# Optimization experiments

Hardware: AMD Instinct MI355X
Metric: run time of the kernel (lower is better)

Reference implementation:

```python
import jax, jax.numpy as jnp
import numpy as np


def setup_inputs() -> dict:
    key = jax.random.key(0)
    ks = jax.random.split(key, 6)
    B, S, H = 4, 256, 768            # batch, subword seq len, BERT hidden
    N = 128                          # token_num (word-level units)
    HID, L = 1024, 16                # MLP hidden, label count
    all_hidden = jax.random.normal(ks[0], (B, S, H), dtype=jnp.float32)
    starts = jax.random.randint(ks[1], (B, N), 0, S)
    W1 = jax.random.normal(ks[2], (4 * H, HID), dtype=jnp.float32) * 0.02
    b1 = jnp.zeros((HID,), dtype=jnp.float32)
    W2 = jax.random.normal(ks[3], (HID, L), dtype=jnp.float32) * 0.02
    b2 = jnp.zeros((L,), dtype=jnp.float32)
    return {"all_hidden": all_hidden, "starts": starts,
            "W1": W1, "b1": b1, "W2": W2, "b2": b2}


def reference(all_hidden, starts, W1, b1, W2, b2):
    # Span gather: con_repr[b, n, :] = all_hidden[b, starts[b, n], :]
    con = jnp.take_along_axis(all_hidden, starts[:, :, None], axis=1)  # [B, N, H]
    B, N, H = con.shape
    a = jnp.broadcast_to(con[:, :, None, :], (B, N, N, H))  # ext_row
    c = jnp.broadcast_to(con[:, None, :, :], (B, N, N, H))  # ext_column
    table = jnp.concatenate([a, c, a - c, a * c], axis=-1)   # [B, N, N, 4H]
    hid = jnp.tanh(jnp.einsum('bijf,fh->bijh', table, W1) + b1)
    out = jnp.einsum('bijh,hl->bijl', hid, W2) + b2          # [B, N, N, L]
    return out
```

## Files before the change

### kernel.cpp

```cpp
#include <hip/hip_runtime.h>
#include <hip/hip_bf16.h>

typedef __attribute__((ext_vector_type(8))) short short8;
typedef __attribute__((ext_vector_type(8))) unsigned short ushort8;
typedef __attribute__((ext_vector_type(4))) float floatx4;
typedef __attribute__((ext_vector_type(16))) float floatx16;
typedef __attribute__((ext_vector_type(4))) unsigned int uint4v;
typedef __attribute__((ext_vector_type(2))) unsigned int uint2v;

#define DEVINL static __device__ __forceinline__

DEVINL float b2f(unsigned short s){ union{unsigned u; float f;} v; v.u=((unsigned)s)<<16; return v.f; }
DEVINL unsigned fbits(float f){ union{float f; unsigned u;} v; v.f=f; return v.u; }
DEVINL unsigned pack2(float f0, float f1){
  return __builtin_amdgcn_perm(fbits(f1)+0x8000u, fbits(f0)+0x8000u, 0x07060302u);
}
DEVINL float tanh_fast(float v){
  float ax = fabsf(v);
  float ex = __expf(-2.f*ax);
  float th = (1.f - ex)*__builtin_amdgcn_rcpf(1.f + ex);
  return copysignf(th, v);
}

constexpr int Sc=256, Hc=768, Nc=128, HIDc=1024, Lc=16;

__global__ __launch_bounds__(256) void k_gather(const float* __restrict__ AH,
                                                const int* __restrict__ ST,
                                                unsigned short* __restrict__ con){
  int row = blockIdx.x;
  int b = row >> 7;
  int st = ST[row];
  const float* src = AH + ((size_t)(b*Sc + st))*Hc;
  unsigned short* dst = con + (size_t)row*Hc;
  int t = threadIdx.x;
  if (t < 192) {
    float4 v = reinterpret_cast<const float4*>(src)[t];
    uint2v o = { pack2(v.x, v.y), pack2(v.z, v.w) };
    *reinterpret_cast<uint2v*>(dst + 4*t) = o;
  }
}

__global__ __launch_bounds__(256) void k_w1m(const float* __restrict__ W1,
                                             unsigned short* __restrict__ w1mF){
  int sid = blockIdx.x*256 + threadIdx.x;
  int l = sid & 63, kc = (sid >> 6) % 48, ht = sid / (48*64);
  int k = kc*16 + (l >> 5)*8;
  int h = ht*32 + (l & 31);
  const float* wp = W1 + (size_t)(2304 + k)*1024 + h;
  uint4v d;
  d[0] = pack2(wp[0],      wp[1024]);
  d[1] = pack2(wp[2*1024], wp[3*1024]);
  d[2] = pack2(wp[4*1024], wp[5*1024]);
  d[3] = pack2(wp[6*1024], wp[7*1024]);
  *reinterpret_cast<uint4v*>(w1mF + (size_t)sid*8) = d;
}

__global__ __launch_bounds__(256) void k_w2t(const float* __restrict__ W2,
                                             unsigned short* __restrict__ w2F2){
  int gid = blockIdx.x*256 + threadIdx.x;
  int l = gid & 63, chunk = gid >> 6;
  int row = l & 31, s = l >> 5;
  unsigned u[4];
  #pragma unroll
  for (int p = 0; p < 4; ++p) {
    int e0 = 2*p, e1 = 2*p + 1;
    int h0 = chunk*16 + 4*s + (e0 & 3) + 8*(e0 >> 2);
    int h1 = chunk*16 + 4*s + (e1 & 3) + 8*(e1 >> 2);
    float v0 = (row < 16) ? W2[(size_t)h0*Lc + row] : 0.f;
    float v1 = (row < 16) ? W2[(size_t)h1*Lc + row] : 0.f;
    u[p] = pack2(v0, v1);
  }
  uint4v d = { u[0], u[1], u[2], u[3] };
  *reinterpret_cast<uint4v*>(w2F2 + (size_t)gid*8) = d;
}

__global__ __launch_bounds__(256) void k_wpq(const float* __restrict__ W1,
                                             unsigned short* __restrict__ wPQF){
  int sid = blockIdx.x*256 + threadIdx.x;
  int lane = sid & 63, kcq = (sid >> 6) % 24, ht = sid / (24*64);
  int col = lane & 15, seg = lane >> 4;
  int hp = ht*16 + col;
  int kb = kcq*32 + seg*8;
  uint4v d;
  if (hp < 1024) {
    const float* w0 = W1 + (size_t)kb*1024 + hp;
    const float* wd = W1 + (size_t)(1536+kb)*1024 + hp;
    d[0] = pack2(w0[0]+wd[0],           w0[1024]+wd[1024]);
    d[1] = pack2(w0[2*1024]+wd[2*1024], w0[3*1024]+wd[3*1024]);
    d[2] = pack2(w0[4*1024]+wd[4*1024], w0[5*1024]+wd[5*1024]);
    d[3] = pack2(w0[6*1024]+wd[6*1024], w0[7*1024]+wd[7*1024]);
  } else {
    int hq = hp - 1024;
    const float* wc = W1 + (size_t)(768+kb)*1024 + hq;
    const float* wd = W1 + (size_t)(1536+kb)*1024 + hq;
    d[0] = pack2(wc[0]-wd[0],           wc[1024]-wd[1024]);
    d[1] = pack2(wc[2*1024]-wd[2*1024], wc[3*1024]-wd[3*1024]);
    d[2] = pack2(wc[4*1024]-wd[4*1024], wc[5*1024]-wd[5*1024]);
    d[3] = pack2(wc[6*1024]-wd[6*1024], wc[7*1024]-wd[7*1024]);
  }
  *reinterpret_cast<uint4v*>(wPQF + (size_t)sid*8) = d;
}

__global__ __launch_bounds__(256) void k_pq(const unsigned short* __restrict__ con,
                                            const unsigned short* __restrict__ wPQF,
                                            float* __restrict__ P, float* __restrict__ Q){
  int rg = blockIdx.x >> 4, hg = blockIdx.x & 15;
  int t = threadIdx.x, w = t >> 6, lane = t & 63;
  int colh = lane & 15, rseg = lane >> 4;
  floatx4 zero = {0.f,0.f,0.f,0.f};
  floatx4 acc[2][2] = {{zero,zero},{zero,zero}};
  const unsigned short* a0p = con + (size_t)(rg*32 + colh)*Hc + rseg*8;
  const unsigned short* a1p = a0p + 16*Hc;
  const unsigned short* b0p = wPQF + (((size_t)((hg*8 + w*2)*24)) << 9) + (lane << 3);
  const unsigned short* b1p = b0p + (24 << 9);
  #pragma unroll
  for (int kc = 0; kc < 24; ++kc) {
    short8 af0 = *reinterpret_cast<const short8*>(a0p + kc*32);
    short8 af1 = *reinterpret_cast<const short8*>(a1p + kc*32);
    short8 bf0 = *reinterpret_cast<const short8*>(b0p + ((size_t)kc << 9));
    short8 bf1 = *reinterpret_cast<const short8*>(b1p + ((size_t)kc << 9));
    acc[0][0] = __builtin_amdgcn_mfma_f32_16x16x32_bf16(af0, bf0, acc[0][0], 0,0,0);
    acc[0][1] = __builtin_amdgcn_mfma_f32_16x16x32_bf16(af0, bf1, acc[0][1], 0,0,0);
    acc[1][0] = __builtin_amdgcn_mfma_f32_16x16x32_bf16(af1, bf0, acc[1][0], 0,0,0);
    acc[1][1] = __builtin_amdgcn_mfma_f32_16x16x32_bf16(af1, bf1, acc[1][1], 0,0,0);
  }
  #pragma unroll
  for (int m = 0; m < 2; ++m)
    #pragma unroll
    for (int n = 0; n < 2; ++n)
      #pragma unroll
      for (int rr = 0; rr < 4; ++rr) {
        int row = rg*32 + m*16 + rseg*4 + rr;
        int hp = hg*128 + w*32 + n*16 + colh;
        float val = acc[m][n][rr];
        if (hg < 8) P[(size_t)row*HIDc + hp] = val;
        else        Q[(size_t)row*HIDc + (hp - 1024)] = val;
      }
}

__global__ __launch_bounds__(256, 2) void k_main(const unsigned short* __restrict__ con,
    const unsigned short* __restrict__ w1mF, const unsigned short* __restrict__ w2F2,
    const float* __restrict__ P, const float* __restrict__ Q, const float* __restrict__ b1,
    const float* __restrict__ b2v, float* __restrict__ out){
  __shared__ float a_row[768];
  __shared__ float Pi_lds[1024];
  __shared__ __align__(16) unsigned short A_lds[2][4][64][8];
  __shared__ __align__(16) float red[16][64][4];

  int bid = blockIdx.x, jh = bid & 1, bi = bid >> 1;
  int b = bi >> 7, i = bi & 127, bN = b*128;
  int t = threadIdx.x, w = t >> 6, lane = t & 63;
  int col32 = lane & 31, hi5 = lane >> 5;

  int kc2A = t >> 7, jtA = (t >> 6) & 1;
  int jstage = jh*64 + jtA*32 + col32;
  int koffA = kc2A*16 + hi5*8;
  const unsigned short* conA = con + (size_t)(bN + jstage)*Hc + koffA;
  unsigned short* Awr0 = &A_lds[0][kc2A*2 + jtA][lane][0];
  unsigned short* Awr1 = &A_lds[1][kc2A*2 + jtA][lane][0];

  if (t < 96) {
    ushort8 c8 = *reinterpret_cast<const ushort8*>(con + (size_t)(bN + i)*Hc + t*8);
    #pragma unroll
    for (int e = 0; e < 8; ++e) a_row[t*8 + e] = b2f((unsigned short)c8[e]);
  }
  {
    float4 p4 = reinterpret_cast<const float4*>(P + (size_t)(bN + i)*HIDc)[t];
    float4 b4 = reinterpret_cast<const float4*>(b1)[t];
    float4 s4 = { p4.x + b4.x, p4.y + b4.y, p4.z + b4.z, p4.w + b4.w };
    *reinterpret_cast<float4*>(&Pi_lds[4*t]) = s4;
  }

  floatx16 acc2_0, acc2_1;
  #pragma unroll
  for (int r = 0; r < 16; ++r) { acc2_0[r] = 0.f; acc2_1[r] = 0.f; }
  __syncthreads();

#define LOADWX(S0,S1,S2,S3, KR) { \
  size_t o_ = ((size_t)((KR)*2)) << 9; \
  S0 = *reinterpret_cast<const ushort8*>(w1p0 + o_); \
  S1 = *reinterpret_cast<const ushort8*>(w1p0 + o_ + 512); \
  S2 = *reinterpret_cast<const ushort8*>(w1p1 + o_); \
  S3 = *reinterpret_cast<const ushort8*>(w1p1 + o_ + 512); }

#define LOADCAV(CA, AV0, AV1, KR) { \
  int k_ = (KR) <= 23 ? (KR) : 23; \
  CA  = *reinterpret_cast<const ushort8*>(conA + k_*32); \
  AV0 = *reinterpret_cast<const floatx4*>(&a_row[k_*32 + koffA]); \
  AV1 = *reinterpret_cast<const floatx4*>(&a_row[k_*32 + koffA + 4]); }

#define PACKWRITE(DST, CA, AV0, AV1) { \
  uint4v dA_; \
  dA_[0] = pack2(AV0[0]*b2f(CA[0]), AV0[1]*b2f(CA[1])); \
  dA_[1] = pack2(AV0[2]*b2f(CA[2]), AV0[3]*b2f(CA[3])); \
  dA_[2] = pack2(AV1[0]*b2f(CA[4]), AV1[1]*b2f(CA[5])); \
  dA_[3] = pack2(AV1[2]*b2f(CA[6]), AV1[3]*b2f(CA[7])); \
  *reinterpret_cast<uint4v*>(DST) = dA_; }

#define MFMA8(BUF, S0,S1,S2,S3) { \
  short8 y00 = *reinterpret_cast<const short8*>(&A_lds[BUF][0][lane][0]); \
  short8 y01 = *reinterpret_cast<const short8*>(&A_lds[BUF][1][lane][0]); \
  short8 y10 = *reinterpret_cast<const short8*>(&A_lds[BUF][2][lane][0]); \
  short8 y11 = *reinterpret_cast<const short8*>(&A_lds[BUF][3][lane][0]); \
  acc00 = __builtin_amdgcn_mfma_f32_32x32x16_bf16(S0, y00, acc00, 0,0,0); \
  acc01 = __builtin_amdgcn_mfma_f32_32x32x16_bf16(S0, y01, acc01, 0,0,0); \
  acc10 = __builtin_amdgcn_mfma_f32_32x32x16_bf16(S2, y00, acc10, 0,0,0); \
  acc11 = __builtin_amdgcn_mfma_f32_32x32x16_bf16(S2, y01, acc11, 0,0,0); \
  acc00 = __builtin_amdgcn_mfma_f32_32x32x16_bf16(S1, y10, acc00, 0,0,0); \
  acc01 = __builtin_amdgcn_mfma_f32_32x32x16_bf16(S1, y11, acc01, 0,0,0); \
  acc10 = __builtin_amdgcn_mfma_f32_32x32x16_bf16(S3, y10, acc10, 0,0,0); \
  acc11 = __builtin_amdgcn_mfma_f32_32x32x16_bf16(S3, y11, acc11, 0,0,0); }

  for (int hc = 0; hc < 4; ++hc) {
    floatx16 acc00, acc01, acc10, acc11;
    #pragma unroll
    for (int r = 0; r < 16; ++r) { acc00[r]=0.f; acc01[r]=0.f; acc10[r]=0.f; acc11[r]=0.f; }

    const unsigned short* w1p0 = w1mF + (((size_t)((hc*8 + w*2)*48)) << 9) + (lane << 3);
    const unsigned short* w1p1 = w1p0 + ((size_t)48 << 9);

    ushort8 caE, caO, wxS0, wxS1, wxS2, wxS3, vxS0, vxS1, vxS2, vxS3;
    floatx4 avE0, avE1, avO0, avO1;

    LOADCAV(caE, avE0, avE1, 0);
    LOADCAV(caO, avO0, avO1, 1);
    LOADWX(wxS0, wxS1, wxS2, wxS3, 0);
    LOADWX(vxS0, vxS1, vxS2, vxS3, 1);
    PACKWRITE(Awr0, caE, avE0, avE1);
    __syncthreads();

    for (int krp = 0; krp < 12; ++krp) {
      {
        const int kr = 2*krp;
        LOADCAV(caE, avE0, avE1, kr+2);
        PACKWRITE(Awr1, caO, avO0, avO1);
        MFMA8(0, wxS0, wxS1, wxS2, wxS3);
        if (kr < 22) LOADWX(wxS0, wxS1, wxS2, wxS3, kr+2);
        __syncthreads();
      }
      {
        const int kr = 2*krp + 1;
        if (kr < 23) {
          LOADCAV(caO, avO0, avO1, kr+2);
          PACKWRITE(Awr0, caE, avE0, avE1);
        }
        MFMA8(1, vxS0, vxS1, vxS2, vxS3);
        if (kr < 22) LOADWX(vxS0, vxS1, vxS2, vxS3, kr+2);
        __syncthreads();
      }
    }

    #pragma unroll
    for (int ht = 0; ht < 2; ++ht) {
      int htg = hc*8 + w*2 + ht;
      const unsigned short* w2p = w2F2 + (((size_t)(htg*2)) << 9) + (lane << 3);
      ushort8 wf0 = *reinterpret_cast<const ushort8*>(w2p);
      ushort8 wf1 = *reinterpret_cast<const ushort8*>(w2p + 512);
      int hbase = htg*32 + 4*hi5;
      #pragma unroll
      for (int jt = 0; jt < 2; ++jt) {
        const floatx16& a = (ht==0) ? (jt==0 ? acc00 : acc01)
                                    : (jt==0 ? acc10 : acc11);
        floatx16& a2 = (jt==0) ? acc2_0 : acc2_1;
        const float* qrow = Q + (size_t)(bN + jh*64 + jt*32 + col32)*HIDc + hbase;
        unsigned hfu[2][4];
        #pragma unroll
        for (int q = 0; q < 4; ++q) {
          floatx4 qv = *reinterpret_cast<const floatx4*>(qrow + 8*q);
          floatx4 pf = *reinterpret_cast<const floatx4*>(&Pi_lds[hbase + 8*q]);
          float t0 = tanh_fast(a[q*4+0] + pf[0] + qv[0]);
          float t1 = tanh_fast(a[q*4+1] + pf[1] + qv[1]);
          float t2 = tanh_fast(a[q*4+2] + pf[2] + qv[2]);
          float t3 = tanh_fast(a[q*4+3] + pf[3] + qv[3]);
          hfu[q >> 1][(q & 1)*2 + 0] = pack2(t0, t1);
          hfu[q >> 1][(q & 1)*2 + 1] = pack2(t2, t3);
        }
        union { uint4v u; short8 s; } f0, f1;
        f0.u[0]=hfu[0][0]; f0.u[1]=hfu[0][1]; f0.u[2]=hfu[0][2]; f0.u[3]=hfu[0][3];
        f1.u[0]=hfu[1][0]; f1.u[1]=hfu[1][1]; f1.u[2]=hfu[1][2]; f1.u[3]=hfu[1][3];
        a2 = __builtin_amdgcn_mfma_f32_32x32x16_bf16(wf0, f0.s, a2, 0,0,0);
        a2 = __builtin_amdgcn_mfma_f32_32x32x16_bf16(wf1, f1.s, a2, 0,0,0);
      }
    }
  }
#undef LOADWX
#undef LOADCAV
#undef PACKWRITE
#undef MFMA8

  #pragma unroll
  for (int q = 0; q < 2; ++q) {
    floatx4 v0 = { acc2_0[q*4+0], acc2_0[q*4+1], acc2_0[q*4+2], acc2_0[q*4+3] };
    floatx4 v1 = { acc2_1[q*4+0], acc2_1[q*4+1], acc2_1[q*4+2], acc2_1[q*4+3] };
    *reinterpret_cast<floatx4*>(&red[(w*2 + 0)*2 + q][lane][0]) = v0;
    *reinterpret_cast<floatx4*>(&red[(w*2 + 1)*2 + q][lane][0]) = v1;
  }
  __syncthreads();
  {
    int jtR = w & 1, qR = w >> 1;
    floatx4 s = {0.f,0.f,0.f,0.f};
    #pragma unroll
    for (int src = 0; src < 4; ++src) {
      floatx4 v = *reinterpret_cast<const floatx4*>(&red[(src*2 + jtR)*2 + qR][lane][0]);
      s[0]+=v[0]; s[1]+=v[1]; s[2]+=v[2]; s[3]+=v[3];
    }
    int jout = jh*64 + jtR*32 + col32;
    int Lb = 8*qR + 4*hi5;
    float* op = out + ((size_t)bi*Nc + jout)*Lc + Lb;
    #pragma unroll
    for (int c = 0; c < 4; ++c) op[c] = s[c] + b2v[Lb + c];
  }
}

extern "C" void kernel_launch(void* const* d_in, const int* in_sizes, int n_in,
                              void* d_out, int out_size, void* d_ws, size_t ws_size,
                              hipStream_t stream) {
  const float* AH = (const float*)d_in[0];
  const int*   ST = (const int*)d_in[1];
  const float* W1 = (const float*)d_in[2];
  const float* b1 = (const float*)d_in[3];
  const float* W2 = (const float*)d_in[4];
  const float* b2 = (const float*)d_in[5];
  float* out = (float*)d_out;

  char* ws = (char*)d_ws;
  unsigned short* con  = (unsigned short*)ws;
  unsigned short* w1mF = (unsigned short*)(ws +   786432);
  unsigned short* wPQF = (unsigned short*)(ws +  2359296);
  float* P = (float*)(ws + 5505024);
  float* Q = (float*)(ws + 7602176);
  unsigned short* w2F2 = (unsigned short*)(ws + 9699328);

  k_gather<<<512, 256, 0, stream>>>(AH, ST, con);
  k_w1m<<<384, 256, 0, stream>>>(W1, w1mF);
  k_w2t<<<16, 256, 0, stream>>>(W2, w2F2);
  k_wpq<<<768, 256, 0, stream>>>(W1, wPQF);
  k_pq<<<256, 256, 0, stream>>>(con, wPQF, P, Q);
  k_main<<<1024, 256, 0, stream>>>(con, w1mF, w2F2, P, Q, b1, b2, out);
}
```

Before: 169.1 us.

## Merge prep kernels, use hardware bf16 pack, simplify tanh

The four preprocessing kernels (gather, W1 mid-block repack, W2 transpose, P/Q weight fold) become one kernel dispatched by block index range, which saves three launches and their gaps. In the main kernel, the bf16 packing of the product tile and the tanh outputs now uses the v_cvt_pk_bf16_f32 instruction instead of manual integer rounding and permute. tanh is rewritten as 1-2/(1+exp2(2x*log2e)), which drops the abs and copysign. The cvt instruction rounds to nearest even, so results can differ slightly, and the new tanh may lose accuracy or hit overflow edge cases for large inputs.

```diff
diff --git a/kernel.cpp b/kernel.cpp
--- a/kernel.cpp
+++ b/kernel.cpp
@@ -15,90 +15,91 @@
 DEVINL unsigned pack2(float f0, float f1){
   return __builtin_amdgcn_perm(fbits(f1)+0x8000u, fbits(f0)+0x8000u, 0x07060302u);
 }
+DEVINL unsigned cvt_pk(float lo, float hi){
+  unsigned r;
+  asm("v_cvt_pk_bf16_f32 %0, %1, %2" : "=v"(r) : "v"(lo), "v"(hi));
+  return r;
+}
 DEVINL float tanh_fast(float v){
-  float ax = fabsf(v);
-  float ex = __expf(-2.f*ax);
-  float th = (1.f - ex)*__builtin_amdgcn_rcpf(1.f + ex);
-  return copysignf(th, v);
+  float ex = __builtin_amdgcn_exp2f(v * 2.885390081777927f);
+  return 1.f - 2.f*__builtin_amdgcn_rcpf(1.f + ex);
 }
 
 constexpr int Sc=256, Hc=768, Nc=128, HIDc=1024, Lc=16;
 
-__global__ __launch_bounds__(256) void k_gather(const float* __restrict__ AH,
-                                                const int* __restrict__ ST,
-                                                unsigned short* __restrict__ con){
-  int row = blockIdx.x;
-  int b = row >> 7;
-  int st = ST[row];
-  const float* src = AH + ((size_t)(b*Sc + st))*Hc;
-  unsigned short* dst = con + (size_t)row*Hc;
-  int t = threadIdx.x;
-  if (t < 192) {
-    float4 v = reinterpret_cast<const float4*>(src)[t];
-    uint2v o = { pack2(v.x, v.y), pack2(v.z, v.w) };
-    *reinterpret_cast<uint2v*>(dst + 4*t) = o;
-  }
-}
-
-__global__ __launch_bounds__(256) void k_w1m(const float* __restrict__ W1,
-                                             unsigned short* __restrict__ w1mF){
-  int sid = blockIdx.x*256 + threadIdx.x;
-  int l = sid & 63, kc = (sid >> 6) % 48, ht = sid / (48*64);
-  int k = kc*16 + (l >> 5)*8;
-  int h = ht*32 + (l & 31);
-  const float* wp = W1 + (size_t)(2304 + k)*1024 + h;
-  uint4v d;
-  d[0] = pack2(wp[0],      wp[1024]);
-  d[1] = pack2(wp[2*1024], wp[3*1024]);
-  d[2] = pack2(wp[4*1024], wp[5*1024]);
-  d[3] = pack2(wp[6*1024], wp[7*1024]);
-  *reinterpret_cast<uint4v*>(w1mF + (size_t)sid*8) = d;
-}
-
-__global__ __launch_bounds__(256) void k_w2t(const float* __restrict__ W2,
-                                             unsigned short* __restrict__ w2F2){
-  int gid = blockIdx.x*256 + threadIdx.x;
-  int l = gid & 63, chunk = gid >> 6;
-  int row = l & 31, s = l >> 5;
-  unsigned u[4];
-  #pragma unroll
-  for (int p = 0; p < 4; ++p) {
-    int e0 = 2*p, e1 = 2*p + 1;
-    int h0 = chunk*16 + 4*s + (e0 & 3) + 8*(e0 >> 2);
-    int h1 = chunk*16 + 4*s + (e1 & 3) + 8*(e1 >> 2);
-    float v0 = (row < 16) ? W2[(size_t)h0*Lc + row] : 0.f;
-    float v1 = (row < 16) ? W2[(size_t)h1*Lc + row] : 0.f;
-    u[p] = pack2(v0, v1);
-  }
-  uint4v d = { u[0], u[1], u[2], u[3] };
-  *reinterpret_cast<uint4v*>(w2F2 + (size_t)gid*8) = d;
-}
-
-__global__ __launch_bounds__(256) void k_wpq(const float* __restrict__ W1,
-                                             unsigned short* __restrict__ wPQF){
-  int sid = blockIdx.x*256 + threadIdx.x;
-  int lane = sid & 63, kcq = (sid >> 6) % 24, ht = sid / (24*64);
-  int col = lane & 15, seg = lane >> 4;
-  int hp = ht*16 + col;
-  int kb = kcq*32 + seg*8;
-  uint4v d;
-  if (hp < 1024) {
-    const float* w0 = W1 + (size_t)kb*1024 + hp;
-    const float* wd = W1 + (size_t)(1536+kb)*1024 + hp;
-    d[0] = pack2(w0[0]+wd[0],           w0[1024]+wd[1024]);
-    d[1] = pack2(w0[2*1024]+wd[2*1024], w0[3*1024]+wd[3*1024]);
-    d[2] = pack2(w0[4*1024]+wd[4*1024], w0[5*1024]+wd[5*1024]);
-    d[3] = pack2(w0[6*1024]+wd[6*1024], w0[7*1024]+wd[7*1024]);
+__global__ __launch_bounds__(256) void k_prep(const float* __restrict__ AH,
+                                              const int* __restrict__ ST,
+                                              const float* __restrict__ W1,
+                                              const float* __restrict__ W2,
+                                              unsigned short* __restrict__ con,
+                                              unsigned short* __restrict__ w1mF,
+                                              unsigned short* __restrict__ w2F2,
+                                              unsigned short* __restrict__ wPQF){
+  int bid = blockIdx.x, t = threadIdx.x;
+  if (bid < 512) {
+    int row = bid;
+    int b = row >> 7;
+    int st = ST[row];
+    const float* src = AH + ((size_t)(b*Sc + st))*Hc;
+    unsigned short* dst = con + (size_t)row*Hc;
+    if (t < 192) {
+      float4 v = reinterpret_cast<const float4*>(src)[t];
+      uint2v o = { pack2(v.x, v.y), pack2(v.z, v.w) };
+      *reinterpret_cast<uint2v*>(dst + 4*t) = o;
+    }
+  } else if (bid < 896) {
+    int sid = (bid - 512)*256 + t;
+    int l = sid & 63, kc = (sid >> 6) % 48, ht = sid / (48*64);
+    int k = kc*16 + (l >> 5)*8;
+    int h = ht*32 + (l & 31);
+    const float* wp = W1 + (size_t)(2304 + k)*1024 + h;
+    uint4v d;
+    d[0] = pack2(wp[0],      wp[1024]);
+    d[1] = pack2(wp[2*1024], wp[3*1024]);
+    d[2] = pack2(wp[4*1024], wp[5*1024]);
+    d[3] = pack2(wp[6*1024], wp[7*1024]);
+    *reinterpret_cast<uint4v*>(w1mF + (size_t)sid*8) = d;
+  } else if (bid < 912) {
+    int gid = (bid - 896)*256 + t;
+    int l = gid & 63, chunk = gid >> 6;
+    int row = l & 31, s = l >> 5;
+    unsigned u[4];
+    #pragma unroll
+    for (int p = 0; p < 4; ++p) {
+      int e0 = 2*p, e1 = 2*p + 1;
+      int h0 = chunk*16 + 4*s + (e0 & 3) + 8*(e0 >> 2);
+      int h1 = chunk*16 + 4*s + (e1 & 3) + 8*(e1 >> 2);
+      float v0 = (row < 16) ? W2[(size_t)h0*Lc + row] : 0.f;
+      float v1 = (row < 16) ? W2[(size_t)h1*Lc + row] : 0.f;
+      u[p] = pack2(v0, v1);
+    }
+    uint4v d = { u[0], u[1], u[2], u[3] };
+    *reinterpret_cast<uint4v*>(w2F2 + (size_t)gid*8) = d;
   } else {
-    int hq = hp - 1024;
-    const float* wc = W1 + (size_t)(768+kb)*1024 + hq;
-    const float* wd = W1 + (size_t)(1536+kb)*1024 + hq;
-    d[0] = pack2(wc[0]-wd[0],           wc[1024]-wd[1024]);
-    d[1] = pack2(wc[2*1024]-wd[2*1024], wc[3*1024]-wd[3*1024]);
-    d[2] = pack2(wc[4*1024]-wd[4*1024], wc[5*1024]-wd[5*1024]);
-    d[3] = pack2(wc[6*1024]-wd[6*1024], wc[7*1024]-wd[7*1024]);
-  }
-  *reinterpret_cast<uint4v*>(wPQF + (size_t)sid*8) = d;
+    int sid = (bid - 912)*256 + t;
+    int lane = sid & 63, kcq = (sid >> 6) % 24, ht = sid / (24*64);
+    int col = lane & 15, seg = lane >> 4;
+    int hp = ht*16 + col;
+    int kb = kcq*32 + seg*8;
+    uint4v d;
+    if (hp < 1024) {
+      const float* w0 = W1 + (size_t)kb*1024 + hp;
+      const float* wd = W1 + (size_t)(1536+kb)*1024 + hp;
+      d[0] = pack2(w0[0]+wd[0],           w0[1024]+wd[1024]);
+      d[1] = pack2(w0[2*1024]+wd[2*1024], w0[3*1024]+wd[3*1024]);
+      d[2] = pack2(w0[4*1024]+wd[4*1024], w0[5*1024]+wd[5*1024]);
+      d[3] = pack2(w0[6*1024]+wd[6*1024], w0[7*1024]+wd[7*1024]);
+    } else {
+      int hq = hp - 1024;
+      const float* wc = W1 + (size_t)(768+kb)*1024 + hq;
+      const float* wd = W1 + (size_t)(1536+kb)*1024 + hq;
+      d[0] = pack2(wc[0]-wd[0],           wc[1024]-wd[1024]);
+      d[1] = pack2(wc[2*1024]-wd[2*1024], wc[3*1024]-wd[3*1024]);
+      d[2] = pack2(wc[4*1024]-wd[4*1024], wc[5*1024]-wd[5*1024]);
+      d[3] = pack2(wc[6*1024]-wd[6*1024], wc[7*1024]-wd[7*1024]);
+    }
+    *reinterpret_cast<uint4v*>(wPQF + (size_t)sid*8) = d;
+  }
 }
 
 __global__ __launch_bounds__(256) void k_pq(const unsigned short* __restrict__ con,
@@ -191,10 +192,10 @@
 
 #define PACKWRITE(DST, CA, AV0, AV1) { \
   uint4v dA_; \
-  dA_[0] = pack2(AV0[0]*b2f(CA[0]), AV0[1]*b2f(CA[1])); \
-  dA_[1] = pack2(AV0[2]*b2f(CA[2]), AV0[3]*b2f(CA[3])); \
-  dA_[2] = pack2(AV1[0]*b2f(CA[4]), AV1[1]*b2f(CA[5])); \
-  dA_[3] = pack2(AV1[2]*b2f(CA[6]), AV1[3]*b2f(CA[7])); \
+  dA_[0] = cvt_pk(AV0[0]*b2f(CA[0]), AV0[1]*b2f(CA[1])); \
+  dA_[1] = cvt_pk(AV0[2]*b2f(CA[2]), AV0[3]*b2f(CA[3])); \
+  dA_[2] = cvt_pk(AV1[0]*b2f(CA[4]), AV1[1]*b2f(CA[5])); \
+  dA_[3] = cvt_pk(AV1[2]*b2f(CA[6]), AV1[3]*b2f(CA[7])); \
   *reinterpret_cast<uint4v*>(DST) = dA_; }
 
 #define MFMA8(BUF, S0,S1,S2,S3) { \
@@ -272,8 +273,8 @@
           float t1 = tanh_fast(a[q*4+1] + pf[1] + qv[1]);
           float t2 = tanh_fast(a[q*4+2] + pf[2] + qv[2]);
           float t3 = tanh_fast(a[q*4+3] + pf[3] + qv[3]);
-          hfu[q >> 1][(q & 1)*2 + 0] = pack2(t0, t1);
-          hfu[q >> 1][(q & 1)*2 + 1] = pack2(t2, t3);
+          hfu[q >> 1][(q & 1)*2 + 0] = cvt_pk(t0, t1);
+          hfu[q >> 1][(q & 1)*2 + 1] = cvt_pk(t2, t3);
         }
         union { uint4v u; short8 s; } f0, f1;
         f0.u[0]=hfu[0][0]; f0.u[1]=hfu[0][1]; f0.u[2]=hfu[0][2]; f0.u[3]=hfu[0][3];
@@ -331,10 +332,7 @@
   float* Q = (float*)(ws + 7602176);
   unsigned short* w2F2 = (unsigned short*)(ws + 9699328);
 
-  k_gather<<<512, 256, 0, stream>>>(AH, ST, con);
-  k_w1m<<<384, 256, 0, stream>>>(W1, w1mF);
-  k_w2t<<<16, 256, 0, stream>>>(W2, w2F2);
-  k_wpq<<<768, 256, 0, stream>>>(W1, wPQF);
+  k_prep<<<1680, 256, 0, stream>>>(AH, ST, W1, W2, con, w1mF, w2F2, wPQF);
   k_pq<<<256, 256, 0, stream>>>(con, wPQF, P, Q);
   k_main<<<1024, 256, 0, stream>>>(con, w1mF, w2F2, P, Q, b1, b2, out);
 }
```

Result: faster. 156.1 us (-7.7%).
